# Performance work log

Measured on AMD Instinct MI355X. Metric: run time of the kernel, lower is better.

Reference implementation:

```python
import jax, jax.numpy as jnp
import numpy as np

B, C, H, W = 16, 96, 96, 96
K, N, R, CR = 4, 8, 6, 12  # scan dirs, d_state, dt_rank, SE hidden


def channel_ln(x, g, b, eps=1e-6):
    # LayerNorm over channel dim (channel_first)
    mu = jnp.mean(x, axis=1, keepdims=True)
    var = jnp.var(x, axis=1, keepdims=True)
    return (x - mu) * jax.lax.rsqrt(var + eps) * g[None, :, None, None] + b[None, :, None, None]


def conv1x1(x, w, b):
    return jnp.einsum('bchw,dc->bdhw', x, w) + b[None, :, None, None]


def ss2d(x, xproj_w, dtproj_w, dtproj_b, A_logs, Ds, g, bta):
    # 4-direction selective scan (VMamba SS2D core). x: (B,C,H,W)
    Bq, Cq, Hq, Wq = x.shape
    L = Hq * Wq
    xf = x.reshape(Bq, Cq, L)
    xt = jnp.transpose(x, (0, 1, 3, 2)).reshape(Bq, Cq, L)
    xs = jnp.stack([xf, xt, xf[..., ::-1], xt[..., ::-1]], axis=1)  # (B,K,C,L)
    x_dbl = jnp.einsum('bkcl,kdc->bkdl', xs, xproj_w)  # (B,K,R+2N,L)
    dts, Bs, Cs = jnp.split(x_dbl, [R, R + N], axis=2)
    delta = jax.nn.softplus(jnp.einsum('bkrl,kcr->bkcl', dts, dtproj_w) + dtproj_b[None, :, :, None])
    A = -jnp.exp(A_logs)  # (K,C,N)
    u_t = jnp.moveaxis(xs, -1, 0)   # (L,B,K,C)
    d_t = jnp.moveaxis(delta, -1, 0)
    B_t = jnp.moveaxis(Bs, -1, 0)   # (L,B,K,N)
    C_t = jnp.moveaxis(Cs, -1, 0)
    h0 = jnp.zeros((Bq, K, Cq, N), x.dtype)

    @jax.checkpoint
    def step(h, inp):
        u, d, Bv, Cv = inp
        dA = jnp.exp(d[..., None] * A)                      # (B,K,C,N)
        h = dA * h + (d * u)[..., None] * Bv[:, :, None, :]
        return h, jnp.sum(h * Cv[:, :, None, :], axis=-1)   # (B,K,C)

    _, ys = jax.lax.scan(step, h0, (u_t, d_t, B_t, C_t))
    ys = jnp.moveaxis(ys, 0, -1) + Ds[None, :, :, None] * xs  # (B,K,C,L)

    def untrans(yk):
        return jnp.transpose(yk.reshape(Bq, Cq, Wq, Hq), (0, 1, 3, 2)).reshape(Bq, Cq, L)

    out = ys[:, 0] + untrans(ys[:, 1]) + ys[:, 2, :, ::-1] + untrans(ys[:, 3][..., ::-1])
    return channel_ln(out.reshape(Bq, Cq, Hq, Wq), g, bta)


def block_forward(x, ln_g, ln_b, p1_w, p1_b, p2in_w, p2in_b, dw_w, dw_b,
                  xproj_w, dtproj_w, dtproj_b, A_logs, Ds, ssln_g, ssln_b,
                  p2n_g, p2n_b, ca_w1, ca_b1, ca_w2, ca_b2, block_idx):
    h = channel_ln(x, ln_g, ln_b)
    a = jax.nn.silu(conv1x1(h, p1_w, p1_b))
    z = conv1x1(h, p2in_w, p2in_b)
    z = jax.lax.conv_general_dilated(z, dw_w, (1, 1), 'SAME',
                                     dimension_numbers=('NCHW', 'OIHW', 'NCHW'),
                                     feature_group_count=z.shape[1]) + dw_b[None, :, None, None]
    z = jax.nn.silu(z)
    if block_idx % 2 == 0:
        z = jnp.transpose(z, (0, 1, 3, 2))
    else:
        z = z[:, :, ::-1, ::-1]
    z = ss2d(z, xproj_w, dtproj_w, dtproj_b, A_logs, Ds, ssln_g, ssln_b)
    if block_idx % 2 == 0:
        z = jnp.transpose(z, (0, 1, 3, 2))
    else:
        z = z[:, :, ::-1, ::-1]
    z = channel_ln(z, p2n_g, p2n_b)
    y = a * z
    # channel attention (SE)
    s = jnp.mean(y, axis=(2, 3))  # (B,C)
    att = jax.nn.sigmoid(jnp.einsum('cr,br->bc', ca_w2,
                                    jax.nn.silu(jnp.einsum('rc,bc->br', ca_w1, s) + ca_b1)) + ca_b2)
    return x + y * att[:, :, None, None]


def local_mamba(x, params, block_idx):
    b, c, h, w = x.shape
    h2, w2 = h // 2, w // 2
    qs = jnp.stack([x[:, :, :h2, :w2], x[:, :, :h2, w2:],
                    x[:, :, h2:, :w2], x[:, :, h2:, w2:]])  # (4,B,C,h2,w2)
    fn = lambda q, *p: block_forward(q, *p, block_idx)
    outs = jax.vmap(fn)(qs, *params)
    top = jnp.concatenate([outs[0], outs[1]], axis=3)
    bot = jnp.concatenate([outs[2], outs[3]], axis=3)
    return jnp.concatenate([top, bot], axis=2)


def setup_inputs() -> dict:
    key = jax.random.key(0)
    ks = jax.random.split(key, 12)
    rn = lambda k, shape, s=1.0: jax.random.normal(k, shape, jnp.float32) * s
    return dict(
        x=rn(ks[0], (B, C, H, W)),
        ln_g=jnp.ones((4, C)), ln_b=jnp.zeros((4, C)),
        p1_w=rn(ks[1], (4, C, C), C ** -0.5), p1_b=jnp.zeros((4, C)),
        p2in_w=rn(ks[2], (4, C, C), C ** -0.5), p2in_b=jnp.zeros((4, C)),
        dw_w=rn(ks[3], (4, C, 1, 3, 3), 1.0 / 3.0), dw_b=jnp.zeros((4, C)),
        xproj_w=rn(ks[4], (4, K, R + 2 * N, C), C ** -0.5),
        dtproj_w=rn(ks[5], (4, K, C, R), R ** -0.5),
        dtproj_b=rn(ks[6], (4, K, C), 0.1),
        A_logs=jax.random.uniform(ks[7], (4, K, C, N), jnp.float32, 0.0, 1.0),
        Ds=jnp.ones((4, K, C)),
        ssln_g=jnp.ones((4, C)), ssln_b=jnp.zeros((4, C)),
        p2n_g=jnp.ones((4, C)), p2n_b=jnp.zeros((4, C)),
        ca_w1=rn(ks[8], (4, CR, C), C ** -0.5), ca_b1=jnp.zeros((4, CR)),
        ca_w2=rn(ks[9], (4, C, CR), CR ** -0.5), ca_b2=jnp.zeros((4, C)),
        block_idx=0,
    )


def reference(x, ln_g, ln_b, p1_w, p1_b, p2in_w, p2in_b, dw_w, dw_b,
              xproj_w, dtproj_w, dtproj_b, A_logs, Ds, ssln_g, ssln_b,
              p2n_g, p2n_b, ca_w1, ca_b1, ca_w2, ca_b2, block_idx):
    params = (ln_g, ln_b, p1_w, p1_b, p2in_w, p2in_b, dw_w, dw_b,
              xproj_w, dtproj_w, dtproj_b, A_logs, Ds, ssln_g, ssln_b,
              p2n_g, p2n_b, ca_w1, ca_b1, ca_w2, ca_b2)
    return local_mamba(x, params, block_idx)
```

## Files before the change

### kernel.cpp

```cpp
#include <hip/hip_runtime.h>
#include <hip/hip_bf16.h>

#define BQ 16
#define CN 96
#define HQ 48
#define LL 2304
#define NK 4
#define RR 6
#define NNS 8
#define DPJ 22
#define CRr 12
#define LOG2E 1.4426950408889634f

using bf16 = __hip_bfloat16;

typedef __attribute__((ext_vector_type(8))) short bf16x8;
typedef __attribute__((ext_vector_type(4))) float f32x4;

__device__ __forceinline__ float b2f(bf16 v) { return __bfloat162float(v); }
__device__ __forceinline__ bf16  f2b(float v){ return __float2bfloat16(v); }
__device__ __forceinline__ float bflo(unsigned u){ return __uint_as_float(u << 16); }
__device__ __forceinline__ float bfhi(unsigned u){ return __uint_as_float(u & 0xffff0000u); }
__device__ __forceinline__ float sigf(float x){ return 1.f / (1.f + __expf(-x)); }
__device__ __forceinline__ float siluf(float x){ return x / (1.f + __expf(-x)); }
__device__ __forceinline__ unsigned packbf(float a, float b){
    unsigned lo = (unsigned)__builtin_bit_cast(unsigned short, f2b(a));
    unsigned hi = (unsigned)__builtin_bit_cast(unsigned short, f2b(b));
    return lo | (hi << 16);
}
__device__ __forceinline__ unsigned rot16(unsigned u){ return (u >> 16) | (u << 16); }
__device__ __forceinline__ void unpack8(uint4 v, float* f){
    f[0]=bflo(v.x); f[1]=bfhi(v.x); f[2]=bflo(v.y); f[3]=bfhi(v.y);
    f[4]=bflo(v.z); f[5]=bfhi(v.z); f[6]=bflo(v.w); f[7]=bfhi(v.w);
}
__device__ __forceinline__ void unpack4(uint2 v, float* f){
    f[0]=bflo(v.x); f[1]=bfhi(v.x); f[2]=bflo(v.y); f[3]=bfhi(v.y);
}
__device__ __forceinline__ float fexp2(float x){
#if __has_builtin(__builtin_amdgcn_exp2f)
    return __builtin_amdgcn_exp2f(x);
#else
    return __expf(x * 0.6931471805599453f);
#endif
}
__device__ __forceinline__ float qxor(float v, int ctrl_b1){
    int x;
    if (ctrl_b1) x = __builtin_amdgcn_mov_dpp(__float_as_int(v), 0xB1, 0xF, 0xF, true);
    else         x = __builtin_amdgcn_mov_dpp(__float_as_int(v), 0x4E, 0xF, 0xF, true);
    return __int_as_float(x);
}

__global__ __launch_bounds__(192) void k_lnconv(
    const float* __restrict__ x, const float* __restrict__ ln_g, const float* __restrict__ ln_b,
    const float* __restrict__ p1w, const float* __restrict__ p1b,
    const float* __restrict__ p2w, const float* __restrict__ p2b,
    bf16* __restrict__ a_out, bf16* __restrict__ z0_out)
{
    const int hh2 = blockIdx.x;
    const int b = blockIdx.y, q = blockIdx.z;
    const int h0 = (q >> 1) * HQ, w0 = (q & 1) * HQ;
    const int tid = threadIdx.x;
    const int qb = q * BQ + b;

    __shared__ alignas(16) bf16 wl2[192 * 104];
    __shared__ alignas(16) bf16 hn2[96 * 104];
    __shared__ float mu[96], rs[96];
    __shared__ float pmu[192], pv2[192];
    __shared__ float biasLds[192];
    __shared__ float gl[96], bl[96];

    for (int t = tid; t < 192 * 24; t += 192) {
        int row = t / 24, c4 = (t % 24) * 4;
        const float* srcw = (row < 96) ? &p1w[(q * CN + row) * CN + c4]
                                       : &p2w[(q * CN + (row - 96)) * CN + c4];
        float4 wv = *reinterpret_cast<const float4*>(srcw);
        uint2 pk; pk.x = packbf(wv.x, wv.y); pk.y = packbf(wv.z, wv.w);
        *reinterpret_cast<uint2*>(&wl2[row * 104 + c4]) = pk;
    }
    if (tid < 192)
        biasLds[tid] = (tid < 96) ? p1b[q * CN + tid] : p2b[q * CN + (tid - 96)];
    if (tid < 96) { gl[tid] = ln_g[q * CN + tid]; bl[tid] = ln_b[q * CN + tid]; }
    for (int t = tid; t < CN * 24; t += 192) {
        int c = t / 24, v = t % 24;
        int row = v / 12, col = (v % 12) * 4;
        int p = row * 48 + col;
        float4 xv = *reinterpret_cast<const float4*>(
            &x[((b * CN + c) * 96 + h0 + 2 * hh2 + row) * 96 + w0 + col]);
        hn2[p * 104 + c]       = f2b(xv.x);
        hn2[(p + 1) * 104 + c] = f2b(xv.y);
        hn2[(p + 2) * 104 + c] = f2b(xv.z);
        hn2[(p + 3) * 104 + c] = f2b(xv.w);
    }
    __syncthreads();
    {
        int p = tid % 96, half = tid / 96;
        const bf16* hp = &hn2[p * 104 + half * 48];
        float s = 0.f, s2 = 0.f;
        #pragma unroll
        for (int c8 = 0; c8 < 48; c8 += 8) {
            float f[8]; unpack8(*reinterpret_cast<const uint4*>(hp + c8), f);
            #pragma unroll
            for (int i = 0; i < 8; ++i) { s += f[i]; s2 += f[i] * f[i]; }
        }
        pmu[half * 96 + p] = s; pv2[half * 96 + p] = s2;
    }
    __syncthreads();
    if (tid < 96) {
        float s = pmu[tid] + pmu[96 + tid];
        float s2 = pv2[tid] + pv2[96 + tid];
        float m = s * (1.f / 96.f);
        float var = s2 * (1.f / 96.f) - m * m;
        mu[tid] = m; rs[tid] = rsqrtf(var + 1e-6f);
    }
    __syncthreads();
    for (int t = tid; t < 96 * 12; t += 192) {
        int p = t / 12, c8 = (t % 12) * 8;
        float f[8]; unpack8(*reinterpret_cast<const uint4*>(&hn2[p * 104 + c8]), f);
        float m = mu[p], r = rs[p];
        unsigned ou[4];
        #pragma unroll
        for (int i = 0; i < 8; i += 2) {
            float v0 = (f[i]     - m) * r * gl[c8 + i]     + bl[c8 + i];
            float v1 = (f[i + 1] - m) * r * gl[c8 + i + 1] + bl[c8 + i + 1];
            ou[i >> 1] = packbf(v0, v1);
        }
        uint4 ov; ov.x = ou[0]; ov.y = ou[1]; ov.z = ou[2]; ov.w = ou[3];
        *reinterpret_cast<uint4*>(&hn2[p * 104 + c8]) = ov;
    }
    __syncthreads();
    const int w = tid >> 6;
    const int l = tid & 63;
    const int lr = l & 15;
    const int lq = l >> 4;
    f32x4 acc[4][6];
    #pragma unroll
    for (int m = 0; m < 4; ++m)
        #pragma unroll
        for (int n = 0; n < 6; ++n)
            acc[m][n] = (f32x4){0.f, 0.f, 0.f, 0.f};
    #pragma unroll
    for (int k0 = 0; k0 < 96; k0 += 32) {
        bf16x8 afr[4], bfr[6];
        #pragma unroll
        for (int m = 0; m < 4; ++m)
            afr[m] = *reinterpret_cast<const bf16x8*>(
                &wl2[(w * 64 + m * 16 + lr) * 104 + k0 + lq * 8]);
        #pragma unroll
        for (int n = 0; n < 6; ++n)
            bfr[n] = *reinterpret_cast<const bf16x8*>(
                &hn2[(n * 16 + lr) * 104 + k0 + lq * 8]);
        #pragma unroll
        for (int m = 0; m < 4; ++m)
            #pragma unroll
            for (int n = 0; n < 6; ++n)
                acc[m][n] = __builtin_amdgcn_mfma_f32_16x16x32_bf16(
                    afr[m], bfr[n], acc[m][n], 0, 0, 0);
    }
    #pragma unroll
    for (int m = 0; m < 4; ++m) {
        const int Rbase = w * 64 + m * 16 + lq * 4;
        #pragma unroll
        for (int n = 0; n < 6; ++n) {
            const int col = n * 16 + lr;
            const int colin = (col >= 48) ? (col - 48) : col;
            const int lbase = (2 * hh2 + (col >= 48 ? 1 : 0)) * 48 + colin;
            #pragma unroll
            for (int r = 0; r < 4; ++r) {
                const int R = Rbase + r;
                const bool isA = R < 96;
                const int d = isA ? R : R - 96;
                float v = acc[m][n][r] + biasLds[R];
                if (isA) v = siluf(v);
                bf16* dst = isA ? a_out : z0_out;
                dst[(size_t)(qb * CN + d) * LL + lbase] = f2b(v);
            }
        }
    }
}

__global__ __launch_bounds__(256) void k_dwconv(
    const bf16* __restrict__ z0, const float* __restrict__ dww, const float* __restrict__ dwb,
    const int* __restrict__ bidx, bf16* __restrict__ zt, bf16* __restrict__ ztT)
{
    const int c = blockIdx.x, b = blockIdx.y, q = blockIdx.z;
    const int tid = threadIdx.x;
    const int base = ((q * BQ + b) * CN + c) * LL;
    __shared__ float zin[50 * 50];
    __shared__ float zo[48 * 49];
    if (tid < 196) {
        int idx;
        if (tid < 50)       idx = tid;
        else if (tid < 100) idx = 49 * 50 + (tid - 50);
        else if (tid < 148) idx = (tid - 99) * 50;
        else                idx = (tid - 147) * 50 + 49;
        zin[idx] = 0.f;
    }
    for (int t = tid; t < 288; t += 256) {
        uint4 v = *reinterpret_cast<const uint4*>(&z0[base + t * 8]);
        float f[8]; unpack8(v, f);
        int e0 = t * 8, row = e0 / 48, col = e0 % 48;
        float* dst = &zin[(row + 1) * 50 + col + 1];
        #pragma unroll
        for (int i = 0; i < 8; ++i) dst[i] = f[i];
    }
    float wk[9];
    #pragma unroll
    for (int i = 0; i < 9; ++i) wk[i] = dww[(q * CN + c) * 9 + i];
    const float bias = dwb[q * CN + c];
    __syncthreads();
    for (int t = tid; t < LL; t += 256) {
        int hh = t / 48, ww = t % 48;
        const float* z0r = &zin[hh * 50 + ww];
        float s = bias;
        s = fmaf(wk[0], z0r[0],        s);
        s = fmaf(wk[1], z0r[1],        s);
        s = fmaf(wk[2], z0r[2],        s);
        s = fmaf(wk[3], z0r[50],       s);
        s = fmaf(wk[4], z0r[51],       s);
        s = fmaf(wk[5], z0r[52],       s);
        s = fmaf(wk[6], z0r[100],      s);
        s = fmaf(wk[7], z0r[101],      s);
        s = fmaf(wk[8], z0r[102],      s);
        zo[hh * 49 + ww] = siluf(s);
    }
    __syncthreads();
    const bool even = ((bidx[0] & 1) == 0);
    for (int t = tid; t < LL; t += 256) {
        int i = t / 48, j = t % 48;
        float vz, vzT;
        if (even) { vz = zo[j * 49 + i];               vzT = zo[i * 49 + j]; }
        else      { vz = zo[(47 - i) * 49 + (47 - j)]; vzT = zo[(47 - j) * 49 + (47 - i)]; }
        zt[base + t]  = f2b(vz);
        ztT[base + t] = f2b(vzT);
    }
}

__global__ __launch_bounds__(256) void k_xdbl(
    const bf16* __restrict__ zt, const bf16* __restrict__ ztT,
    const float* __restrict__ xprojw, bf16* __restrict__ xdbl)
{
    const int lt = blockIdx.x, k = blockIdx.y, qb = blockIdx.z;
    const int tid = threadIdx.x;
    const int l0 = lt * 192;
    const int q = qb >> 4;
    __shared__ alignas(16) bf16 ul[CN * 200];
    __shared__ alignas(16) bf16 wl[CN * 24];
    const bf16* __restrict__ src = (k & 1) ? ztT : zt;
    const bool rev = (k >= 2);
    for (int t = tid; t < CN * 24; t += 256) {
        int cc = t / 24, j0 = (t % 24) * 8;
        uint4 v;
        if (!rev) {
            v = *reinterpret_cast<const uint4*>(&src[(size_t)(qb * CN + cc) * LL + l0 + j0]);
        } else {
            v = *reinterpret_cast<const uint4*>(&src[(size_t)(qb * CN + cc) * LL + (LL - (l0 + j0) - 8)]);
            uint4 r; r.x = rot16(v.w); r.y = rot16(v.z); r.z = rot16(v.y); r.w = rot16(v.x);
            v = r;
        }
        *reinterpret_cast<uint4*>(&ul[cc * 200 + j0]) = v;
    }
    for (int t = tid; t < DPJ * CN; t += 256) {
        int d = t / CN, c = t % CN;
        wl[c * 24 + d] = f2b(xprojw[(q * NK + k) * DPJ * CN + t]);
    }
    __syncthreads();
    if (tid < 176) {
        const int dp = tid / 16, lg = tid % 16;
        const int d0 = dp * 2, llp = lg * 12;
        float acc0[12], acc1[12];
        #pragma unroll
        for (int j = 0; j < 12; ++j) { acc0[j] = 0.f; acc1[j] = 0.f; }
        for (int c = 0; c < CN; ++c) {
            unsigned wv = *reinterpret_cast<const unsigned*>(&wl[c * 24 + d0]);
            float w0 = bflo(wv), w1 = bfhi(wv);
            uint2 ua = *reinterpret_cast<const uint2*>(&ul[c * 200 + llp]);
            uint2 ub = *reinterpret_cast<const uint2*>(&ul[c * 200 + llp + 4]);
            uint2 uc = *reinterpret_cast<const uint2*>(&ul[c * 200 + llp + 8]);
            float uf[12];
            unpack4(ua, uf); unpack4(ub, uf + 4); unpack4(uc, uf + 8);
            #pragma unroll
            for (int j = 0; j < 12; ++j) {
                acc0[j] = fmaf(w0, uf[j], acc0[j]);
                acc1[j] = fmaf(w1, uf[j], acc1[j]);
            }
        }
        int ob = (qb * NK + k) * DPJ * LL + l0 + llp;
        uint2 o0a, o0b, o0c, o1a, o1b, o1c;
        o0a.x = packbf(acc0[0], acc0[1]);  o0a.y = packbf(acc0[2], acc0[3]);
        o0b.x = packbf(acc0[4], acc0[5]);  o0b.y = packbf(acc0[6], acc0[7]);
        o0c.x = packbf(acc0[8], acc0[9]);  o0c.y = packbf(acc0[10], acc0[11]);
        o1a.x = packbf(acc1[0], acc1[1]);  o1a.y = packbf(acc1[2], acc1[3]);
        o1b.x = packbf(acc1[4], acc1[5]);  o1b.y = packbf(acc1[6], acc1[7]);
        o1c.x = packbf(acc1[8], acc1[9]);  o1c.y = packbf(acc1[10], acc1[11]);
        *reinterpret_cast<uint2*>(&xdbl[ob + d0 * LL])           = o0a;
        *reinterpret_cast<uint2*>(&xdbl[ob + d0 * LL + 4])       = o0b;
        *reinterpret_cast<uint2*>(&xdbl[ob + d0 * LL + 8])       = o0c;
        *reinterpret_cast<uint2*>(&xdbl[ob + (d0 + 1) * LL])     = o1a;
        *reinterpret_cast<uint2*>(&xdbl[ob + (d0 + 1) * LL + 4]) = o1b;
        *reinterpret_cast<uint2*>(&xdbl[ob + (d0 + 1) * LL + 8]) = o1c;
    }
}


#define SCAN_BARRIER() asm volatile("s_waitcnt lgkmcnt(0)\n\ts_barrier" ::: "memory")

#define UWORD(NUA, IDX) (((IDX) & 3) == 0 ? NUA[(IDX) >> 2].x : \
                         ((IDX) & 3) == 1 ? NUA[(IDX) >> 2].y : \
                         ((IDX) & 3) == 2 ? NUA[(IDX) >> 2].z : NUA[(IDX) >> 2].w)

#define ROT3(v) (v) = ((v) == 2) ? 0 : ((v) + 1)

__global__ __launch_bounds__(384) void k_scan(
    const bf16* __restrict__ zt, const bf16* __restrict__ ztT,
    const bf16* __restrict__ xdbl,
    const float* __restrict__ dtw_g, const float* __restrict__ dtb_g,
    const float* __restrict__ Alog_g, const float* __restrict__ Ds_g,
    bf16* __restrict__ ys)
{
    const int bid = blockIdx.x;
    const int ch2 = bid & 1, k = (bid >> 1) & 3, qb = bid >> 3, q = qb >> 4;
    const int qk = q * NK + k;
    const int tid = threadIdx.x;
    const bool isScan = (tid < 192);
    const int lt = isScan ? tid : (tid - 192);
    const int ca = lt >> 2, p = lt & 3;
    const int c = ch2 * 48 + ca;

    __shared__ float dd3[3][48 * 52];
    __shared__ float xr3[3][6 * 52];
    __shared__ float bcv3[3][48 * 16];

    const bf16* __restrict__ src = (k & 1) ? ztT : zt;
    const bool rev = (k >= 2);
    const int ja = p * 12;

    float wdt[6] = {0.f, 0.f, 0.f, 0.f, 0.f, 0.f};
    float dtbc = 0.f;
    if (!isScan) {
        const float* wp = dtw_g + (size_t)qk * CN * RR + c * RR;
        float2 wa = *reinterpret_cast<const float2*>(wp);
        float2 wb = *reinterpret_cast<const float2*>(wp + 2);
        float2 wc = *reinterpret_cast<const float2*>(wp + 4);
        wdt[0] = wa.x; wdt[1] = wa.y; wdt[2] = wb.x; wdt[3] = wb.y; wdt[4] = wc.x; wdt[5] = wc.y;
        dtbc = dtb_g[qk * CN + c];
    }
    const bool xload = (!isScan) && (lt < 132);
    const int vr = lt / 6, jx = (lt % 6) * 8;
    const bf16* gx = xdbl + (size_t)(qb * NK + k) * (DPJ * LL) + (size_t)vr * LL + jx;
    int bccol = 0;
    if (vr >= 6) {
        int v = vr - 6;
        int n = v & 7;
        bccol = (n >> 1) * 4 + ((v >= 8) ? 2 : 0) + (n & 1);
    }

    float A0L = 0.f, A1L = 0.f, Dc = 0.f;
    if (isScan) {
        A0L = -__expf(Alog_g[((size_t)qk * CN + c) * NNS + 2 * p])     * LOG2E;
        A1L = -__expf(Alog_g[((size_t)qk * CN + c) * NNS + 2 * p + 1]) * LOG2E;
        Dc = Ds_g[qk * CN + c];
    }
    float h0 = 0.f, h1 = 0.f;
    const bf16* gu = src + (size_t)(qb * CN + c) * LL + (rev ? (LL - 48) : 0);
    const int ustep = rev ? -48 : 48;
    bf16* yp = ys + (size_t)(qb * NK + k) * (CN * LL) + (size_t)c * LL;

    #define COMMIT_BLOCK(PXV, XRB, BCB) do {                                          \
        if (xload) {                                                                  \
            float g[8]; unpack8(PXV, g);                                              \
            if (vr < 6) {                                                             \
                *reinterpret_cast<float4*>(&(XRB)[vr * 52 + jx])                      \
                    = make_float4(g[0], g[1], g[2], g[3]);                            \
                *reinterpret_cast<float4*>(&(XRB)[vr * 52 + jx + 4])                  \
                    = make_float4(g[4], g[5], g[6], g[7]);                            \
            } else {                                                                  \
                _Pragma("unroll")                                                     \
                for (int i = 0; i < 8; ++i) (BCB)[(jx + i) * 16 + bccol] = g[i];      \
            }                                                                         \
        }                                                                             \
    } while (0)

    #define DELTA_BLOCK(XRB, DDB) do {                                                \
        float acc[12];                                                                \
        _Pragma("unroll")                                                             \
        for (int i = 0; i < 12; ++i) acc[i] = dtbc;                                   \
        _Pragma("unroll")                                                             \
        for (int r = 0; r < 6; ++r) {                                                 \
            float4 d0 = *reinterpret_cast<const float4*>(&(XRB)[r * 52 + ja]);        \
            float4 d1 = *reinterpret_cast<const float4*>(&(XRB)[r * 52 + ja + 4]);    \
            float4 d2 = *reinterpret_cast<const float4*>(&(XRB)[r * 52 + ja + 8]);    \
            float wr_ = wdt[r];                                                       \
            acc[0] = fmaf(wr_, d0.x, acc[0]);  acc[1] = fmaf(wr_, d0.y, acc[1]);      \
            acc[2] = fmaf(wr_, d0.z, acc[2]);  acc[3] = fmaf(wr_, d0.w, acc[3]);      \
            acc[4] = fmaf(wr_, d1.x, acc[4]);  acc[5] = fmaf(wr_, d1.y, acc[5]);      \
            acc[6] = fmaf(wr_, d1.z, acc[6]);  acc[7] = fmaf(wr_, d1.w, acc[7]);      \
            acc[8] = fmaf(wr_, d2.x, acc[8]);  acc[9] = fmaf(wr_, d2.y, acc[9]);      \
            acc[10] = fmaf(wr_, d2.z, acc[10]); acc[11] = fmaf(wr_, d2.w, acc[11]);   \
        }                                                                             \
        _Pragma("unroll")                                                             \
        for (int i = 0; i < 12; ++i) {                                                \
            float a = acc[i];                                                         \
            acc[i] = (a > 15.f) ? a : __logf(1.f + __expf(a));                        \
        }                                                                             \
        float4* dp = reinterpret_cast<float4*>(&(DDB)[ca * 52 + ja]);                 \
        dp[0] = make_float4(acc[0], acc[1], acc[2], acc[3]);                          \
        dp[1] = make_float4(acc[4], acc[5], acc[6], acc[7]);                          \
        dp[2] = make_float4(acc[8], acc[9], acc[10], acc[11]);                        \
    } while (0)

    uint4 u_a[6], u_b[6];
    uint4 px_a = {0,0,0,0}, px_b = {0,0,0,0}, px1 = {0,0,0,0};
    if (isScan) {
        #pragma unroll
        for (int i = 0; i < 6; ++i) u_a[i] = *reinterpret_cast<const uint4*>(gu + i * 8);
        gu += ustep;
        #pragma unroll
        for (int i = 0; i < 6; ++i) u_b[i] = *reinterpret_cast<const uint4*>(gu + i * 8);
        gu += ustep;
    } else {
        uint4 px0 = {0,0,0,0};
        if (xload) {
            px0  = *reinterpret_cast<const uint4*>(gx);
            px1  = *reinterpret_cast<const uint4*>(gx + 48);
            px_a = *reinterpret_cast<const uint4*>(gx + 96);
            px_b = *reinterpret_cast<const uint4*>(gx + 144);
            gx += 192;
        }
        COMMIT_BLOCK(px0, xr3[0], bcv3[0]);
    }
    SCAN_BARRIER();
    if (!isScan) {
        DELTA_BLOCK(xr3[0], dd3[0]);
        COMMIT_BLOCK(px1, xr3[1], bcv3[1]);
    }
    SCAN_BARRIER();

    int s_cur = 0;
    int d_idx = 1, c_idx = 2;

    #define PROD_BODY(CH, PX) do {                                                    \
        const int chp_ = (CH);                                                        \
        if (chp_ + 2 < 48) COMMIT_BLOCK(PX, xr3[c_idx], bcv3[c_idx]);                 \
        if (chp_ + 4 < 48 && xload) { PX = *reinterpret_cast<const uint4*>(gx); gx += 48; } \
        if (chp_ + 1 < 48) DELTA_BLOCK(xr3[d_idx], dd3[d_idx]);                       \
        ROT3(d_idx); ROT3(c_idx);                                                     \
    } while (0)

    #define SCAN_CHUNK(CH, UC) do {                                                   \
        const int ch_ = (CH);                                                         \
        uint4 nu[6];                                                                  \
        if (!rev) {                                                                   \
            nu[0] = UC[0]; nu[1] = UC[1]; nu[2] = UC[2];                              \
            nu[3] = UC[3]; nu[4] = UC[4]; nu[5] = UC[5];                              \
        } else {                                                                      \
            _Pragma("unroll")                                                         \
            for (int qq = 0; qq < 6; ++qq) {                                          \
                nu[qq].x = rot16(UC[5 - qq].w); nu[qq].y = rot16(UC[5 - qq].z);       \
                nu[qq].z = rot16(UC[5 - qq].y); nu[qq].w = rot16(UC[5 - qq].x);       \
            }                                                                         \
        }                                                                             \
        {                                                                             \
            const int l0 = ch_ * 48;                                                  \
            const float* ddc = &dd3[s_cur][ca * 52];                                  \
            const float* bcc = &bcv3[s_cur][p * 4];                                   \
            _Pragma("unroll")                                                         \
            for (int gg = 0; gg < 6; ++gg) {                                          \
                unsigned pk[4];                                                       \
                _Pragma("unroll")                                                     \
                for (int half = 0; half < 2; ++half) {                                \
                    const int j0 = gg * 8 + half * 4;                                 \
                    float4 d4 = *reinterpret_cast<const float4*>(ddc + j0);           \
                    const float* df = reinterpret_cast<const float*>(&d4);            \
                    _Pragma("unroll")                                                 \
                    for (int s = 0; s < 4; ++s) {                                     \
                        const int j = j0 + s;                                         \
                        const unsigned uwv = UWORD(nu, j >> 1);                       \
                        float u = (j & 1) ? bfhi(uwv) : bflo(uwv);                    \
                        float d = df[s];                                              \
                        float4 bq = *reinterpret_cast<const float4*>(bcc + j * 16);   \
                        float du = d * u;                                             \
                        float dA0 = fexp2(d * A0L);                                   \
                        float dA1 = fexp2(d * A1L);                                   \
                        h0 = fmaf(dA0, h0, du * bq.x);                                \
                        h1 = fmaf(dA1, h1, du * bq.y);                                \
                        float y = fmaf(h0, bq.z, h1 * bq.w);                          \
                        y += qxor(y, 1); y += qxor(y, 0);                             \
                        y = fmaf(Dc, u, y);                                           \
                        unsigned hb = (unsigned)__builtin_bit_cast(unsigned short, f2b(y)); \
                        const int sl = half * 4 + s;                                  \
                        if (sl & 1) pk[sl >> 1] |= hb << 16; else pk[sl >> 1] = hb;   \
                    }                                                                 \
                }                                                                     \
                if (p == 0) {                                                         \
                    uint4 wv4; wv4.x = pk[0]; wv4.y = pk[1]; wv4.z = pk[2]; wv4.w = pk[3]; \
                    *reinterpret_cast<uint4*>(yp + l0 + gg * 8) = wv4;                \
                }                                                                     \
            }                                                                         \
        }                                                                             \
        if (ch_ + 2 < 48) {                                                           \
            _Pragma("unroll")                                                         \
            for (int i = 0; i < 6; ++i) UC[i] = *reinterpret_cast<const uint4*>(gu + i * 8); \
            gu += ustep;                                                              \
        }                                                                             \
        ROT3(s_cur);                                                                  \
    } while (0)

    for (int t = 0; t < 24; ++t) {
        if (isScan) SCAN_CHUNK(2 * t, u_a);
        else        PROD_BODY(2 * t, px_a);
        SCAN_BARRIER();
        if (isScan) SCAN_CHUNK(2 * t + 1, u_b);
        else        PROD_BODY(2 * t + 1, px_b);
        SCAN_BARRIER();
    }

    #undef SCAN_CHUNK
    #undef PROD_BODY
    #undef DELTA_BLOCK
    #undef COMMIT_BLOCK
}

__global__ __launch_bounds__(256) void k_sum(
    const bf16* __restrict__ ys, bf16* __restrict__ s_out)
{
    const int c = blockIdx.x, b = blockIdx.y, q = blockIdx.z;
    const int qb = q * BQ + b;
    const int tid = threadIdx.x;
    __shared__ float t0[48 * 49];
    __shared__ float t2[48 * 49];
    const size_t base0 = ((size_t)(qb * NK + 0) * CN + c) * LL;
    const size_t base1 = ((size_t)(qb * NK + 1) * CN + c) * LL;
    const size_t base2 = ((size_t)(qb * NK + 2) * CN + c) * LL;
    const size_t base3 = ((size_t)(qb * NK + 3) * CN + c) * LL;
    for (int idx = tid; idx < 288; idx += 256) {
        int e0 = idx * 8, h = e0 / 48, w = e0 % 48;
        float f[8];
        unpack8(*reinterpret_cast<const uint4*>(&ys[base0 + e0]), f);
        #pragma unroll
        for (int i = 0; i < 8; ++i) t0[h * 49 + w + i] = f[i];
        unpack8(*reinterpret_cast<const uint4*>(&ys[base2 + e0]), f);
        #pragma unroll
        for (int i = 0; i < 8; ++i) t2[h * 49 + w + i] = f[i];
    }
    __syncthreads();
    const size_t cbase = ((size_t)qb * CN + c) * LL;
    for (int idx = tid; idx < 288; idx += 256) {
        int m0 = idx * 8, ww = m0 / 48, hh = m0 % 48;
        float f1[8], f3[8];
        unpack8(*reinterpret_cast<const uint4*>(&ys[base1 + m0]), f1);
        unpack8(*reinterpret_cast<const uint4*>(&ys[base3 + (LL - 8 - m0)]), f3);
        float o[8];
        #pragma unroll
        for (int i = 0; i < 8; ++i) {
            float v0 = t0[(hh + i) * 49 + ww];
            float v2 = t2[(47 - hh - i) * 49 + (47 - ww)];
            o[i] = v0 + f1[i] + v2 + f3[7 - i];
        }
        uint4 w;
        w.x = packbf(o[0], o[1]); w.y = packbf(o[2], o[3]);
        w.z = packbf(o[4], o[5]); w.w = packbf(o[6], o[7]);
        *reinterpret_cast<uint4*>(&s_out[cbase + m0]) = w;
    }
}

__global__ __launch_bounds__(256) void k_combine(
    const bf16* __restrict__ s_in, const bf16* __restrict__ a_in,
    const float* __restrict__ ssg, const float* __restrict__ ssb,
    const float* __restrict__ png, const float* __restrict__ pnb,
    const int* __restrict__ bidx,
    bf16* __restrict__ y_out, float* __restrict__ s_buf)
{
    const int ww = blockIdx.x, b = blockIdx.y, q = blockIdx.z;
    const int qb = q * BQ + b;
    const int tid = threadIdx.x;
    __shared__ float o[CN * 48];
    __shared__ float mu[48], rs[48];
    __shared__ float pp[192], pp2[192];
    for (int v = tid; v < 576; v += 256) {
        int e0 = v * 8, cc = e0 / 48, hh = e0 % 48;
        float f[8];
        unpack8(*reinterpret_cast<const uint4*>(&s_in[((size_t)qb * CN + cc) * LL + ww * 48 + hh]), f);
        #pragma unroll
        for (int i = 0; i < 8; ++i) o[cc * 48 + hh + i] = f[i];
    }
    __syncthreads();
    if (tid < 192) {
        int hh = tid % 48, part = tid / 48;
        float s = 0.f, s2 = 0.f;
        int c0 = part * 24;
        for (int cc = c0; cc < c0 + 24; ++cc) { float v = o[cc * 48 + hh]; s += v; s2 += v * v; }
        pp[tid] = s; pp2[tid] = s2;
    }
    __syncthreads();
    if (tid < 48) {
        float s = pp[tid] + pp[tid + 48] + pp[tid + 96] + pp[tid + 144];
        float s2 = pp2[tid] + pp2[tid + 48] + pp2[tid + 96] + pp2[tid + 144];
        float m = s * (1.f / 96.f), var = s2 * (1.f / 96.f) - m * m;
        mu[tid] = m; rs[tid] = rsqrtf(var + 1e-6f);
    }
    __syncthreads();
    for (int t = tid; t < CN * 48; t += 256) {
        int cc = t / 48, hh = t % 48;
        o[t] = (o[t] - mu[hh]) * rs[hh] * ssg[q * CN + cc] + ssb[q * CN + cc];
    }
    __syncthreads();
    if (tid < 192) {
        int hh = tid % 48, part = tid / 48;
        float s = 0.f, s2 = 0.f;
        int c0 = part * 24;
        for (int cc = c0; cc < c0 + 24; ++cc) { float v = o[cc * 48 + hh]; s += v; s2 += v * v; }
        pp[tid] = s; pp2[tid] = s2;
    }
    __syncthreads();
    if (tid < 48) {
        float s = pp[tid] + pp[tid + 48] + pp[tid + 96] + pp[tid + 144];
        float s2 = pp2[tid] + pp2[tid + 48] + pp2[tid + 96] + pp2[tid + 144];
        float m = s * (1.f / 96.f), var = s2 * (1.f / 96.f) - m * m;
        mu[tid] = m; rs[tid] = rsqrtf(var + 1e-6f);
    }
    __syncthreads();
    const bool even = ((bidx[0] & 1) == 0);
    if (even) {
        for (int v = tid; v < 576; v += 256) {
            int e0 = v * 8, cc = e0 / 48, hh = e0 % 48;
            size_t oidx = ((size_t)qb * CN + cc) * LL + ww * 48 + hh;
            float af[8];
            unpack8(*reinterpret_cast<const uint4*>(&a_in[oidx]), af);
            float yv[8];
            #pragma unroll
            for (int i = 0; i < 8; ++i) {
                float z2 = (o[cc * 48 + hh + i] - mu[hh + i]) * rs[hh + i] * png[q * CN + cc] + pnb[q * CN + cc];
                yv[i] = af[i] * z2;
                o[cc * 48 + hh + i] = yv[i];
            }
            uint4 w;
            w.x = packbf(yv[0], yv[1]); w.y = packbf(yv[2], yv[3]);
            w.z = packbf(yv[4], yv[5]); w.w = packbf(yv[6], yv[7]);
            *reinterpret_cast<uint4*>(&y_out[oidx]) = w;
        }
    } else {
        for (int t = tid; t < CN * 48; t += 256) {
            int cc = t / 48, hh = t % 48;
            float z2 = (o[t] - mu[hh]) * rs[hh] * png[q * CN + cc] + pnb[q * CN + cc];
            size_t oidx = ((size_t)qb * CN + cc) * LL + (47 - hh) * 48 + (47 - ww);
            float yv = b2f(a_in[oidx]) * z2;
            y_out[oidx] = f2b(yv);
            o[t] = yv;
        }
    }
    __syncthreads();
    if (tid < CN) {
        float s = 0.f;
        for (int j = 0; j < 48; ++j) s += o[tid * 48 + j];
        atomicAdd(&s_buf[qb * CN + tid], s);
    }
}

__global__ __launch_bounds__(256) void k_final(
    const float* __restrict__ x, const bf16* __restrict__ y_in,
    const float* __restrict__ s_buf,
    const float* __restrict__ w1, const float* __restrict__ b1,
    const float* __restrict__ w2, const float* __restrict__ b2,
    float* __restrict__ out)
{
    const int c = blockIdx.x, b = blockIdx.y, q = blockIdx.z;
    const int h0 = (q >> 1) * HQ, w0 = (q & 1) * HQ;
    const int qb = q * BQ + b;
    const int tid = threadIdx.x;
    __shared__ float tl[CRr];
    __shared__ float tpart[16 * CRr];
    __shared__ float attv;
    if (tid < 192) {
        int r = tid % CRr, part = tid / CRr;
        float acc = 0.f;
        const float* wr = w1 + (q * CRr + r) * CN;
        const float* sb = s_buf + qb * CN;
        int c0 = part * 6;
        for (int cc = c0; cc < c0 + 6; ++cc)
            acc = fmaf(wr[cc], sb[cc] * (1.f / (float)LL), acc);
        tpart[part * CRr + r] = acc;
    }
    __syncthreads();
    if (tid < CRr) {
        float acc = b1[q * CRr + tid];
        #pragma unroll
        for (int pt = 0; pt < 16; ++pt) acc += tpart[pt * CRr + tid];
        tl[tid] = siluf(acc);
    }
    __syncthreads();
    if (tid == 0) {
        float acc = b2[q * CN + c];
        #pragma unroll
        for (int r = 0; r < CRr; ++r) acc = fmaf(w2[(q * CN + c) * CRr + r], tl[r], acc);
        attv = sigf(acc);
    }
    __syncthreads();
    const float av = attv;
    const size_t ybase = (size_t)(qb * CN + c) * LL;
    const int xb = (b * CN + c) * 9216 + h0 * 96 + w0;
    for (int t = tid; t < LL / 8; t += 256) {
        int e0 = t * 8;
        int gi = xb + (e0 / 48) * 96 + (e0 % 48);
        uint4 yv = *reinterpret_cast<const uint4*>(&y_in[ybase + e0]);
        float yf[8]; unpack8(yv, yf);
        float4 xa = *reinterpret_cast<const float4*>(&x[gi]);
        float4 xc = *reinterpret_cast<const float4*>(&x[gi + 4]);
        float4 o0 = {xa.x + yf[0]*av, xa.y + yf[1]*av, xa.z + yf[2]*av, xa.w + yf[3]*av};
        float4 o1 = {xc.x + yf[4]*av, xc.y + yf[5]*av, xc.z + yf[6]*av, xc.w + yf[7]*av};
        *reinterpret_cast<float4*>(&out[gi])     = o0;
        *reinterpret_cast<float4*>(&out[gi + 4]) = o1;
    }
}

extern "C" void kernel_launch(void* const* d_in, const int* in_sizes, int n_in,
                              void* d_out, int out_size, void* d_ws, size_t ws_size,
                              hipStream_t stream)
{
    (void)in_sizes; (void)n_in; (void)out_size; (void)ws_size;
    const float* x       = (const float*)d_in[0];
    const float* ln_g    = (const float*)d_in[1];
    const float* ln_b    = (const float*)d_in[2];
    const float* p1_w    = (const float*)d_in[3];
    const float* p1_b    = (const float*)d_in[4];
    const float* p2in_w  = (const float*)d_in[5];
    const float* p2in_b  = (const float*)d_in[6];
    const float* dw_w    = (const float*)d_in[7];
    const float* dw_b    = (const float*)d_in[8];
    const float* xproj_w = (const float*)d_in[9];
    const float* dtproj_w= (const float*)d_in[10];
    const float* dtproj_b= (const float*)d_in[11];
    const float* A_logs  = (const float*)d_in[12];
    const float* Ds      = (const float*)d_in[13];
    const float* ssln_g  = (const float*)d_in[14];
    const float* ssln_b  = (const float*)d_in[15];
    const float* p2n_g   = (const float*)d_in[16];
    const float* p2n_b   = (const float*)d_in[17];
    const float* ca_w1   = (const float*)d_in[18];
    const float* ca_b1   = (const float*)d_in[19];
    const float* ca_w2   = (const float*)d_in[20];
    const float* ca_b2   = (const float*)d_in[21];
    const int*  bidx     = (const int*)d_in[22];
    float* out = (float*)d_out;

    char* ws = (char*)d_ws;
    const size_t off_a    = 0;
    const size_t off_zt   = 28311552;
    const size_t off_ztT  = 56623104;
    const size_t off_xdbl = 84934656;
    const size_t off_ys   = 110886912;
    const size_t off_z0   = off_ys;
    const size_t off_s    = off_zt;
    const size_t off_y    = off_ztT;
    const size_t off_sb   = 224133120;

    bf16*  a_buf   = (bf16*)(ws + off_a);
    bf16*  zt_buf  = (bf16*)(ws + off_zt);
    bf16*  ztT_buf = (bf16*)(ws + off_ztT);
    bf16*  xdbl_buf= (bf16*)(ws + off_xdbl);
    bf16*  ys_buf  = (bf16*)(ws + off_ys);
    bf16*  z0_buf  = (bf16*)(ws + off_z0);
    bf16*  s_sum   = (bf16*)(ws + off_s);
    bf16*  y_buf   = (bf16*)(ws + off_y);
    float* s_buf   = (float*)(ws + off_sb);

    (void)hipMemsetAsync(ws + off_sb, 0, 24576, stream);

    k_lnconv<<<dim3(24, 16, 4), 192, 0, stream>>>(
        x, ln_g, ln_b, p1_w, p1_b, p2in_w, p2in_b, a_buf, z0_buf);
    k_dwconv<<<dim3(96, 16, 4), 256, 0, stream>>>(
        z0_buf, dw_w, dw_b, bidx, zt_buf, ztT_buf);
    k_xdbl<<<dim3(12, 4, 64), 256, 0, stream>>>(
        zt_buf, ztT_buf, xproj_w, xdbl_buf);
    k_scan<<<dim3(512), 384, 0, stream>>>(
        zt_buf, ztT_buf, xdbl_buf, dtproj_w, dtproj_b, A_logs, Ds, ys_buf);
    k_sum<<<dim3(96, 16, 4), 256, 0, stream>>>(
        ys_buf, s_sum);
    k_combine<<<dim3(48, 16, 4), 256, 0, stream>>>(
        s_sum, a_buf, ssln_g, ssln_b, p2n_g, p2n_b, bidx, y_buf, s_buf);
    k_final<<<dim3(96, 16, 4), 256, 0, stream>>>(
        x, y_buf, s_buf, ca_w1, ca_b1, ca_w2, ca_b2, out);
}
```

Before: 632.8 us.

## Compute x_proj projection in k_xdbl with bf16 MFMA instead of scalar FMAs

The x_dbl projection kernel now stages the input tile transposed in LDS (position-major, channel-contiguous) and the weights padded to 32 rows. It computes the 22x192 output tile with mfma_f32_16x16x32_bf16 across four waves. This replaces the per-thread scalar FMA loop, which left 80 of 256 threads idle, with matrix-core work. In exchange, the transposed LDS store is a scattered per-element write, the output stores become scalar bf16 writes, and a third of the MFMA rows are padding.

```diff
diff --git a/kernel.cpp b/kernel.cpp
--- a/kernel.cpp
+++ b/kernel.cpp
@@ -243,10 +243,20 @@
     const int tid = threadIdx.x;
     const int l0 = lt * 192;
     const int q = qb >> 4;
-    __shared__ alignas(16) bf16 ul[CN * 200];
-    __shared__ alignas(16) bf16 wl[CN * 24];
+    __shared__ alignas(16) bf16 ub[192 * 104];
+    __shared__ alignas(16) bf16 wl3[32 * 104];
     const bf16* __restrict__ src = (k & 1) ? ztT : zt;
     const bool rev = (k >= 2);
+
+    for (int t = tid; t < 520; t += 256)
+        reinterpret_cast<unsigned*>(&wl3[22 * 104])[t] = 0u;
+    for (int t = tid; t < DPJ * 24; t += 256) {
+        int d = t / 24, c4 = (t % 24) * 4;
+        float4 wv = *reinterpret_cast<const float4*>(
+            &xprojw[((q * NK + k) * DPJ + d) * CN + c4]);
+        uint2 pk; pk.x = packbf(wv.x, wv.y); pk.y = packbf(wv.z, wv.w);
+        *reinterpret_cast<uint2*>(&wl3[d * 104 + c4]) = pk;
+    }
     for (int t = tid; t < CN * 24; t += 256) {
         int cc = t / 24, j0 = (t % 24) * 8;
         uint4 v;
@@ -257,47 +267,53 @@
             uint4 r; r.x = rot16(v.w); r.y = rot16(v.z); r.z = rot16(v.y); r.w = rot16(v.x);
             v = r;
         }
-        *reinterpret_cast<uint4*>(&ul[cc * 200 + j0]) = v;
-    }
-    for (int t = tid; t < DPJ * CN; t += 256) {
-        int d = t / CN, c = t % CN;
-        wl[c * 24 + d] = f2b(xprojw[(q * NK + k) * DPJ * CN + t]);
-    }
-    __syncthreads();
-    if (tid < 176) {
-        const int dp = tid / 16, lg = tid % 16;
-        const int d0 = dp * 2, llp = lg * 12;
-        float acc0[12], acc1[12];
-        #pragma unroll
-        for (int j = 0; j < 12; ++j) { acc0[j] = 0.f; acc1[j] = 0.f; }
-        for (int c = 0; c < CN; ++c) {
-            unsigned wv = *reinterpret_cast<const unsigned*>(&wl[c * 24 + d0]);
-            float w0 = bflo(wv), w1 = bfhi(wv);
-            uint2 ua = *reinterpret_cast<const uint2*>(&ul[c * 200 + llp]);
-            uint2 ub = *reinterpret_cast<const uint2*>(&ul[c * 200 + llp + 4]);
-            uint2 uc = *reinterpret_cast<const uint2*>(&ul[c * 200 + llp + 8]);
-            float uf[12];
-            unpack4(ua, uf); unpack4(ub, uf + 4); unpack4(uc, uf + 8);
+        const unsigned short* ev = reinterpret_cast<const unsigned short*>(&v);
+        unsigned short* ubs = reinterpret_cast<unsigned short*>(ub);
+        #pragma unroll
+        for (int i = 0; i < 8; ++i) ubs[(j0 + i) * 104 + cc] = ev[i];
+    }
+    __syncthreads();
+    const int w = tid >> 6;
+    const int l = tid & 63;
+    const int lr = l & 15;
+    const int lq = l >> 4;
+    f32x4 acc[2][3];
+    #pragma unroll
+    for (int m = 0; m < 2; ++m)
+        #pragma unroll
+        for (int n = 0; n < 3; ++n)
+            acc[m][n] = (f32x4){0.f, 0.f, 0.f, 0.f};
+    #pragma unroll
+    for (int k0 = 0; k0 < 96; k0 += 32) {
+        bf16x8 afr[2], bfr[3];
+        #pragma unroll
+        for (int m = 0; m < 2; ++m)
+            afr[m] = *reinterpret_cast<const bf16x8*>(
+                &wl3[(m * 16 + lr) * 104 + k0 + lq * 8]);
+        #pragma unroll
+        for (int n = 0; n < 3; ++n)
+            bfr[n] = *reinterpret_cast<const bf16x8*>(
+                &ub[((w * 3 + n) * 16 + lr) * 104 + k0 + lq * 8]);
+        #pragma unroll
+        for (int m = 0; m < 2; ++m)
             #pragma unroll
-            for (int j = 0; j < 12; ++j) {
-                acc0[j] = fmaf(w0, uf[j], acc0[j]);
-                acc1[j] = fmaf(w1, uf[j], acc1[j]);
+            for (int n = 0; n < 3; ++n)
+                acc[m][n] = __builtin_amdgcn_mfma_f32_16x16x32_bf16(
+                    afr[m], bfr[n], acc[m][n], 0, 0, 0);
+    }
+    const size_t obase = (size_t)(qb * NK + k) * (DPJ * LL);
+    #pragma unroll
+    for (int m = 0; m < 2; ++m) {
+        #pragma unroll
+        for (int n = 0; n < 3; ++n) {
+            const int lpos = l0 + (w * 3 + n) * 16 + lr;
+            #pragma unroll
+            for (int r = 0; r < 4; ++r) {
+                const int d = m * 16 + lq * 4 + r;
+                if (d < DPJ)
+                    xdbl[obase + (size_t)d * LL + lpos] = f2b(acc[m][n][r]);
             }
         }
-        int ob = (qb * NK + k) * DPJ * LL + l0 + llp;
-        uint2 o0a, o0b, o0c, o1a, o1b, o1c;
-        o0a.x = packbf(acc0[0], acc0[1]);  o0a.y = packbf(acc0[2], acc0[3]);
-        o0b.x = packbf(acc0[4], acc0[5]);  o0b.y = packbf(acc0[6], acc0[7]);
-        o0c.x = packbf(acc0[8], acc0[9]);  o0c.y = packbf(acc0[10], acc0[11]);
-        o1a.x = packbf(acc1[0], acc1[1]);  o1a.y = packbf(acc1[2], acc1[3]);
-        o1b.x = packbf(acc1[4], acc1[5]);  o1b.y = packbf(acc1[6], acc1[7]);
-        o1c.x = packbf(acc1[8], acc1[9]);  o1c.y = packbf(acc1[10], acc1[11]);
-        *reinterpret_cast<uint2*>(&xdbl[ob + d0 * LL])           = o0a;
-        *reinterpret_cast<uint2*>(&xdbl[ob + d0 * LL + 4])       = o0b;
-        *reinterpret_cast<uint2*>(&xdbl[ob + d0 * LL + 8])       = o0c;
-        *reinterpret_cast<uint2*>(&xdbl[ob + (d0 + 1) * LL])     = o1a;
-        *reinterpret_cast<uint2*>(&xdbl[ob + (d0 + 1) * LL + 4]) = o1b;
-        *reinterpret_cast<uint2*>(&xdbl[ob + (d0 + 1) * LL + 8]) = o1c;
     }
 }
 
```

After: 630.0 us. About the same (-0.4%).
